# Kernel optimization log

Measured on AMD Instinct MI355X. Metric: run time of the kernel, lower is better.

## Reference

```python
import jax, jax.numpy as jnp
import numpy as np

IN_FEATURES = 4096
OUT_FEATURES = 4096
BLOCK_SIZE = 4096
NUM_BLOCKS = 4096
CODEBOOK_SIZE = 256
TOTAL_WEIGHTS = OUT_FEATURES * IN_FEATURES


def setup_inputs() -> dict:
    key = jax.random.key(0)
    k_x, k_cb, k_b, k_idx = jax.random.split(key, 4)
    x = jax.random.normal(k_x, (4, 2048, IN_FEATURES), dtype=jnp.float32)
    codebook = jax.random.normal(k_cb, (NUM_BLOCKS, CODEBOOK_SIZE), dtype=jnp.float32)
    bias = jax.random.normal(k_b, (OUT_FEATURES,), dtype=jnp.float32)
    indices = jax.random.randint(k_idx, (NUM_BLOCKS, BLOCK_SIZE), 0, CODEBOOK_SIZE, dtype=jnp.int64)
    return {"x": x, "codebook": codebook, "bias": bias, "indices": indices}


def reference(x, codebook, bias, indices):
    # weight = codebook[block_idx, indices] : per-block gather of codebook entries
    # codebook: [num_blocks, codebook_size], indices: [num_blocks, block_size]
    w_blocks = jnp.take_along_axis(codebook, indices, axis=1)  # [num_blocks, block_size]
    weight = w_blocks.reshape(-1)[:TOTAL_WEIGHTS].reshape(OUT_FEATURES, IN_FEATURES)
    # F.linear: x @ weight.T + bias
    return jnp.einsum("bsi,oi->bso", x, weight) + bias
```

## Files before the change

kernel.cpp:

```cpp
#include <hip/hip_runtime.h>

typedef __bf16 bf16x8 __attribute__((ext_vector_type(8)));
typedef float f32x4 __attribute__((ext_vector_type(4)));
typedef unsigned short u16x8 __attribute__((ext_vector_type(8)));
typedef int i32x4 __attribute__((ext_vector_type(4)));

#define M_TOT 8192
#define K_TOT 4096
#define N_TOT 4096
#define BM 256
#define BN 256
#define BK 64
#define NT (K_TOT / BK)

__device__ __forceinline__ unsigned short f2bf(float f) {
  union { float f; unsigned int u; } v; v.f = f;
  unsigned int u = v.u;
  return (unsigned short)((u + 0x7FFFu + ((u >> 16) & 1u)) >> 16);
}

__global__ __launch_bounds__(256) void deq_w(const float* __restrict__ cb,
                                             const int* __restrict__ idx,
                                             unsigned short* __restrict__ Wb) {
  size_t base = ((size_t)blockIdx.x * 256 + threadIdx.x) * 8;
  const float* crow = cb + ((base >> 12) << 8);
  i32x4 i0 = *(const i32x4*)(idx + base);
  i32x4 i1 = *(const i32x4*)(idx + base + 4);
  u16x8 o;
#pragma unroll
  for (int j = 0; j < 4; ++j) { o[j] = f2bf(crow[i0[j]]); o[4 + j] = f2bf(crow[i1[j]]); }
  *(u16x8*)(Wb + base) = o;
}

__global__ __launch_bounds__(256) void conv_x(const float* __restrict__ X,
                                              unsigned short* __restrict__ Xc) {
  size_t base = ((size_t)blockIdx.x * 256 + threadIdx.x) * 8;
  f32x4 a = *(const f32x4*)(X + base);
  f32x4 b = *(const f32x4*)(X + base + 4);
  u16x8 o;
#pragma unroll
  for (int j = 0; j < 4; ++j) { o[j] = f2bf(a[j]); o[4 + j] = f2bf(b[j]); }
  *(u16x8*)(Xc + base) = o;
}

#define GLDS16(g, l)                                                      \
  __builtin_amdgcn_global_load_lds(                                       \
      (__attribute__((address_space(1))) void*)(g),                       \
      (__attribute__((address_space(3))) void*)(l), 16, 0, 0)

__global__ __launch_bounds__(512, 2) void gemm8(const unsigned short* __restrict__ A,
                                                const unsigned short* __restrict__ B,
                                                const float* __restrict__ bias,
                                                float* __restrict__ C) {
  __shared__ __attribute__((aligned(128))) char lds[131072];

  const int tid = threadIdx.x;
  const int lane = tid & 63;
  const int wm = (tid >> 6) >> 2;
  const int wn = (tid >> 6) & 3;
  const int lr = lane & 15;

  const int bid = blockIdx.x;
  const int swz = (bid & 7) * 64 + (bid >> 3);
  const int bm = swz >> 4;
  const int bn = swz & 15;

  const unsigned short* Ap = A + (size_t)bm * BM * K_TOT;
  const unsigned short* Bp = B + (size_t)bn * BN * K_TOT;

  const int srow = tid >> 3;
  const int sgcol = (((tid & 7) * 16) ^ ((srow & 7) << 4)) >> 1;
  const int wavebase = (tid & 448) << 4;

  const int cs0 = (((lane >> 4) << 4)) ^ ((lr & 7) << 4);
  const int cs1 = (64 + ((lane >> 4) << 4)) ^ ((lr & 7) << 4);
  const int rowA0 = (wm * 128 + lr) * 128;
  const int rowB0 = 32768 + (wn * 64 + lr) * 128;

#define RD(off) (*(const bf16x8*)(lds + (off)))
#define STAGE(GB, TK, RB, LOFF)                                               \
  { _Pragma("unroll")                                                         \
    for (int ii = 0; ii < 2; ++ii) {                                          \
      GLDS16((GB) + (size_t)((RB) + ii * 64 + srow) * K_TOT + (TK) + sgcol,   \
             lds + (LOFF) + ii * 8192 + wavebase);                            \
    } }
#define BARRIER()                       \
  {                                     \
    asm volatile("" ::: "memory");      \
    __builtin_amdgcn_s_barrier();       \
    asm volatile("" ::: "memory");      \
  }

#define MFMA_Q(MH, AV, BV)                                                    \
  { __builtin_amdgcn_s_setprio(1);                                            \
    _Pragma("unroll")                                                         \
    for (int r = 0; r < 4; ++r) {                                             \
      _Pragma("unroll")                                                       \
      for (int nf = 0; nf < 4; ++nf)                                          \
        acc[(MH) * 4 + r][nf] = __builtin_amdgcn_mfma_f32_16x16x32_bf16(      \
            AV[r], BV[nf], acc[(MH) * 4 + r][nf], 0, 0, 0);                   \
    }                                                                         \
    __builtin_amdgcn_s_setprio(0); }

#define TILE(T, BO, STG_A, STG_B, VMF, DO_BAR)                                    \
  {                                                                               \
    bf16x8 Aa[4], Ab[4], Ac[4], Ad[4], Bx[4], By[4];                              \
    _Pragma("unroll") for (int r = 0; r < 4; ++r)                                 \
        Aa[r] = RD((BO) + rowA0 + r * 2048 + cs0);                                \
    _Pragma("unroll") for (int n = 0; n < 4; ++n)                                 \
        Bx[n] = RD((BO) + rowB0 + n * 2048 + cs0);                                \
    if (STG_A) STAGE(Ap, ((T) + 1) * BK, 0, ((BO) ^ 65536) + 0);                  \
    _Pragma("unroll") for (int r = 0; r < 4; ++r)                                 \
        Ab[r] = RD((BO) + rowA0 + (4 + r) * 2048 + cs0);                          \
    if (STG_A) STAGE(Ap, ((T) + 1) * BK, 128, ((BO) ^ 65536) + 16384);            \
    MFMA_Q(0, Aa, Bx);                                                            \
    _Pragma("unroll") for (int r = 0; r < 4; ++r)                                 \
        Ac[r] = RD((BO) + rowA0 + r * 2048 + cs1);                                \
    _Pragma("unroll") for (int n = 0; n < 4; ++n)                                 \
        By[n] = RD((BO) + rowB0 + n * 2048 + cs1);                                \
    MFMA_Q(1, Ab, Bx);                                                            \
    asm volatile("s_waitcnt lgkmcnt(0)" ::: "memory");                            \
    BARRIER();                                                                    \
    if (STG_B) STAGE(Bp, ((T) + 2) * BK, 0, (BO) + 32768);                        \
    if (STG_B) STAGE(Bp, ((T) + 2) * BK, 128, (BO) + 49152);                      \
    _Pragma("unroll") for (int r = 0; r < 4; ++r)                                 \
        Ad[r] = RD((BO) + rowA0 + (4 + r) * 2048 + cs1);                          \
    MFMA_Q(0, Ac, By);                                                            \
    MFMA_Q(1, Ad, By);                                                            \
    asm volatile("s_waitcnt vmcnt(" VMF ")" ::: "memory");                        \
    if (DO_BAR) BARRIER();                                                        \
  }

  f32x4 acc[8][4] = {};

  STAGE(Bp, 0, 0, 32768);
  STAGE(Bp, 0, 128, 49152);
  STAGE(Ap, 0, 0, 0);
  STAGE(Ap, 0, 128, 16384);
  STAGE(Bp, BK, 0, 65536 + 32768);
  STAGE(Bp, BK, 128, 65536 + 49152);
  asm volatile("s_waitcnt vmcnt(4)" ::: "memory");
  BARRIER();

  for (int t = 0; t < NT - 2; t += 2) {
    TILE(t,     0,     1, 1, "4", 1);
    TILE(t + 1, 65536, 1, 1, "4", 1);
  }
  TILE(NT - 2, 0,     1, 0, "0", 1);
  TILE(NT - 1, 65536, 0, 0, "0", 0);

  const int lg4 = (lane >> 4) << 2;
#pragma unroll
  for (int nf = 0; nf < 4; ++nf) {
    const int col = bn * BN + wn * 64 + nf * 16 + lr;
    const float bv = bias[col];
#pragma unroll
    for (int mf = 0; mf < 8; ++mf) {
      const int row0 = bm * BM + wm * 128 + mf * 16 + lg4;
      float* cp = C + (size_t)row0 * N_TOT + col;
#pragma unroll
      for (int j = 0; j < 4; ++j) cp[(size_t)j * N_TOT] = acc[mf][nf][j] + bv;
    }
  }
#undef RD
#undef STAGE
#undef BARRIER
#undef MFMA_Q
#undef TILE
}

extern "C" void kernel_launch(void* const* d_in, const int* in_sizes, int n_in,
                              void* d_out, int out_size, void* d_ws, size_t ws_size,
                              hipStream_t stream) {
  const float* x    = (const float*)d_in[0];
  const float* cb   = (const float*)d_in[1];
  const float* bias = (const float*)d_in[2];
  const int*   idx  = (const int*)d_in[3];

  float* out = (float*)d_out;

  unsigned short* Wb = (unsigned short*)d_ws;
  unsigned short* Xc = (unsigned short*)((char*)d_ws + (size_t)N_TOT * K_TOT * 2);

  deq_w<<<(N_TOT * (size_t)K_TOT) / (8 * 256), 256, 0, stream>>>(cb, idx, Wb);
  conv_x<<<((size_t)M_TOT * K_TOT) / (8 * 256), 256, 0, stream>>>(x, Xc);
  gemm8<<<512, 512, 0, stream>>>(Xc, Wb, bias, out);
}
```

Measured before the change: 274.1 us.

## Fuse fp32-to-bf16 activation conversion into GEMM A-tile staging

Removes the separate conv_x kernel and has the GEMM load fp32 activations straight from global memory into registers, convert them to bf16, and write them into swizzled LDS. This drops a full pass that wrote and re-read the bf16 copy of X. In exchange the GEMM reads twice as many bytes for A per tile, needs extra registers and VALU conversion work, and loses the async global_load_lds path for A. That could hurt MFMA overlap and occupancy, since the A tile is re-read for each of the 16 column blocks.

```diff
diff --git a/kernel.cpp b/kernel.cpp
--- a/kernel.cpp
+++ b/kernel.cpp
@@ -19,9 +19,9 @@
   return (unsigned short)((u + 0x7FFFu + ((u >> 16) & 1u)) >> 16);
 }
 
-__global__ __launch_bounds__(256) void deq_w(const float* __restrict__ cb,
-                                             const int* __restrict__ idx,
-                                             unsigned short* __restrict__ Wb) {
+__global__ __launch_bounds__(256) void prep(const float* __restrict__ cb,
+                                            const int* __restrict__ idx,
+                                            unsigned short* __restrict__ Wb) {
   size_t base = ((size_t)blockIdx.x * 256 + threadIdx.x) * 8;
   const float* crow = cb + ((base >> 12) << 8);
   i32x4 i0 = *(const i32x4*)(idx + base);
@@ -32,23 +32,12 @@
   *(u16x8*)(Wb + base) = o;
 }
 
-__global__ __launch_bounds__(256) void conv_x(const float* __restrict__ X,
-                                              unsigned short* __restrict__ Xc) {
-  size_t base = ((size_t)blockIdx.x * 256 + threadIdx.x) * 8;
-  f32x4 a = *(const f32x4*)(X + base);
-  f32x4 b = *(const f32x4*)(X + base + 4);
-  u16x8 o;
-#pragma unroll
-  for (int j = 0; j < 4; ++j) { o[j] = f2bf(a[j]); o[4 + j] = f2bf(b[j]); }
-  *(u16x8*)(Xc + base) = o;
-}
-
 #define GLDS16(g, l)                                                      \
   __builtin_amdgcn_global_load_lds(                                       \
       (__attribute__((address_space(1))) void*)(g),                       \
       (__attribute__((address_space(3))) void*)(l), 16, 0, 0)
 
-__global__ __launch_bounds__(512, 2) void gemm8(const unsigned short* __restrict__ A,
+__global__ __launch_bounds__(512, 2) void gemm8(const float* __restrict__ X,
                                                 const unsigned short* __restrict__ B,
                                                 const float* __restrict__ bias,
                                                 float* __restrict__ C) {
@@ -65,8 +54,13 @@
   const int bm = swz >> 4;
   const int bn = swz & 15;
 
-  const unsigned short* Ap = A + (size_t)bm * BM * K_TOT;
   const unsigned short* Bp = B + (size_t)bn * BN * K_TOT;
+
+  const int arow = tid >> 1;
+  const int akh  = tid & 1;
+  const float* Axp = X + ((size_t)(bm * BM + arow)) * K_TOT + akh * 32;
+  const int aswz = (arow & 7) << 4;
+  const int aldsrow = arow * 128;
 
   const int srow = tid >> 3;
   const int sgcol = (((tid & 7) * 16) ^ ((srow & 7) << 4)) >> 1;
@@ -91,6 +85,18 @@
     asm volatile("" ::: "memory");      \
   }
 
+#define ALOADF(KOFF)                                                          \
+  { _Pragma("unroll") for (int q = 0; q < 8; ++q)                             \
+      af32[q] = *(const f32x4*)(Axp + (KOFF) + q * 4); }
+
+#define ACVTW(LOFF)                                                           \
+  { _Pragma("unroll") for (int j = 0; j < 4; ++j) {                           \
+      u16x8 w;                                                                \
+      _Pragma("unroll") for (int e = 0; e < 8; ++e)                           \
+        w[e] = f2bf(af32[j * 2 + (e >> 2)][e & 3]);                           \
+      *(u16x8*)(lds + (LOFF) + aldsrow + ((akh * 64 + j * 16) ^ aswz)) = w;   \
+    } }
+
 #define MFMA_Q(MH, AV, BV)                                                    \
   { __builtin_amdgcn_s_setprio(1);                                            \
     _Pragma("unroll")                                                         \
@@ -102,17 +108,17 @@
     }                                                                         \
     __builtin_amdgcn_s_setprio(0); }
 
-#define TILE(T, BO, STG_A, STG_B, VMF, DO_BAR)                                    \
+#define TILE(T, BO, STG_A, STG_B, VMF, LAST)                                      \
   {                                                                               \
     bf16x8 Aa[4], Ab[4], Ac[4], Ad[4], Bx[4], By[4];                              \
+    f32x4 af32[8];                                                                \
+    if (STG_A) ALOADF(((T) + 1) * BK);                                            \
     _Pragma("unroll") for (int r = 0; r < 4; ++r)                                 \
         Aa[r] = RD((BO) + rowA0 + r * 2048 + cs0);                                \
     _Pragma("unroll") for (int n = 0; n < 4; ++n)                                 \
         Bx[n] = RD((BO) + rowB0 + n * 2048 + cs0);                                \
-    if (STG_A) STAGE(Ap, ((T) + 1) * BK, 0, ((BO) ^ 65536) + 0);                  \
     _Pragma("unroll") for (int r = 0; r < 4; ++r)                                 \
         Ab[r] = RD((BO) + rowA0 + (4 + r) * 2048 + cs0);                          \
-    if (STG_A) STAGE(Ap, ((T) + 1) * BK, 128, ((BO) ^ 65536) + 16384);            \
     MFMA_Q(0, Aa, Bx);                                                            \
     _Pragma("unroll") for (int r = 0; r < 4; ++r)                                 \
         Ac[r] = RD((BO) + rowA0 + r * 2048 + cs1);                                \
@@ -122,32 +128,43 @@
     asm volatile("s_waitcnt lgkmcnt(0)" ::: "memory");                            \
     BARRIER();                                                                    \
     if (STG_B) STAGE(Bp, ((T) + 2) * BK, 0, (BO) + 32768);                        \
+    if (STG_A) {                                                                  \
+      asm volatile("s_waitcnt vmcnt(" VMF ")" ::: "memory");                      \
+      ACVTW((BO) ^ 65536);                                                        \
+    }                                                                             \
     if (STG_B) STAGE(Bp, ((T) + 2) * BK, 128, (BO) + 49152);                      \
     _Pragma("unroll") for (int r = 0; r < 4; ++r)                                 \
         Ad[r] = RD((BO) + rowA0 + (4 + r) * 2048 + cs1);                          \
     MFMA_Q(0, Ac, By);                                                            \
     MFMA_Q(1, Ad, By);                                                            \
-    asm volatile("s_waitcnt vmcnt(" VMF ")" ::: "memory");                        \
-    if (DO_BAR) BARRIER();                                                        \
+    if (!(LAST)) {                                                                \
+      asm volatile("s_waitcnt lgkmcnt(0)" ::: "memory");                          \
+      BARRIER();                                                                  \
+    }                                                                             \
   }
 
   f32x4 acc[8][4] = {};
 
-  STAGE(Bp, 0, 0, 32768);
-  STAGE(Bp, 0, 128, 49152);
-  STAGE(Ap, 0, 0, 0);
-  STAGE(Ap, 0, 128, 16384);
-  STAGE(Bp, BK, 0, 65536 + 32768);
-  STAGE(Bp, BK, 128, 65536 + 49152);
-  asm volatile("s_waitcnt vmcnt(4)" ::: "memory");
-  BARRIER();
+  {
+    f32x4 af32[8];
+    ALOADF(0);
+    STAGE(Bp, 0, 0, 32768);
+    STAGE(Bp, 0, 128, 49152);
+    STAGE(Bp, BK, 0, 65536 + 32768);
+    STAGE(Bp, BK, 128, 65536 + 49152);
+    asm volatile("s_waitcnt vmcnt(8)" ::: "memory");
+    ACVTW(0);
+    asm volatile("s_waitcnt vmcnt(4)" ::: "memory");
+    asm volatile("s_waitcnt lgkmcnt(0)" ::: "memory");
+    BARRIER();
+  }
 
   for (int t = 0; t < NT - 2; t += 2) {
-    TILE(t,     0,     1, 1, "4", 1);
-    TILE(t + 1, 65536, 1, 1, "4", 1);
-  }
-  TILE(NT - 2, 0,     1, 0, "0", 1);
-  TILE(NT - 1, 65536, 0, 0, "0", 0);
+    TILE(t,     0,     1, 1, "2", 0);
+    TILE(t + 1, 65536, 1, 1, "2", 0);
+  }
+  TILE(NT - 2, 0,     1, 0, "0", 0);
+  TILE(NT - 1, 65536, 0, 0, "0", 1);
 
   const int lg4 = (lane >> 4) << 2;
 #pragma unroll
@@ -165,6 +182,8 @@
 #undef RD
 #undef STAGE
 #undef BARRIER
+#undef ALOADF
+#undef ACVTW
 #undef MFMA_Q
 #undef TILE
 }
@@ -180,9 +199,7 @@
   float* out = (float*)d_out;
 
   unsigned short* Wb = (unsigned short*)d_ws;
-  unsigned short* Xc = (unsigned short*)((char*)d_ws + (size_t)N_TOT * K_TOT * 2);
-
-  deq_w<<<(N_TOT * (size_t)K_TOT) / (8 * 256), 256, 0, stream>>>(cb, idx, Wb);
-  conv_x<<<((size_t)M_TOT * K_TOT) / (8 * 256), 256, 0, stream>>>(x, Xc);
-  gemm8<<<512, 512, 0, stream>>>(Xc, Wb, bias, out);
-}
+
+  prep<<<8192, 256, 0, stream>>>(cb, idx, Wb);
+  gemm8<<<512, 512, 0, stream>>>(x, Wb, bias, out);
+}
```

Result: slower. 487.9 us (+78.0%).
